# Optimization experiments

Measured on AMD Instinct MI355X. Metric: run time of the kernel, lower is better.

The kernel has to match this reference:

```python
import jax, jax.numpy as jnp
import numpy as np

OUT, IN = 11008, 4096
B, S = 8, 32


def setup_inputs() -> dict:
    key = jax.random.key(0)
    k_x, k_w, k_s, k_b = jax.random.split(key, 4)
    x = jax.random.normal(k_x, (B, S, IN), dtype=jnp.float32).astype(jnp.float16)
    # int8 weight storage (symmetric quant range [-128, 127])
    w_int8 = jax.random.randint(k_w, (OUT, IN), -128, 128, dtype=jnp.int32).astype(jnp.int8)
    # per-output-channel scale, small positive values typical of int8 quant
    scale = jax.random.uniform(k_s, (OUT,), dtype=jnp.float32) * 0.01 + 1e-4
    bias = (jax.random.normal(k_b, (OUT,), dtype=jnp.float32) * 0.02).astype(jnp.float16)
    return {"x": x, "w_int8": w_int8, "scale": scale, "bias": bias}


def reference(x, w_int8, scale, bias):
    # w_fp[o, i] = int8_weight[o, i] * scale[o]   (on-the-fly dequant)
    w = w_int8.astype(jnp.float32) * scale[:, None]          # [OUT, IN] fp32
    # F.linear: out = x @ w.T + bias, computed in fp32
    out = jnp.einsum('bsi,oi->bso', x.astype(jnp.float32), w) + bias.astype(jnp.float32)
    return out.astype(x.dtype)                                # cast back to x.dtype (fp16)
```

## Files before the change

### kernel.cpp

```cpp
#include <hip/hip_runtime.h>
#include <hip/hip_bf16.h>
#include <stdint.h>

typedef __attribute__((ext_vector_type(8))) __bf16 bf16x8;
typedef __attribute__((ext_vector_type(4))) float f32x4;

constexpr int K_DIM = 4096;
constexpr int N_DIM = 11008;
constexpr int M_DIM = 256;
constexpr int TN = 32;
constexpr int BK = 64;
constexpr int NT = 256;
constexpr int KTILES = K_DIM / BK;

__device__ __forceinline__ void gload_lds16(const __bf16* gptr, __bf16* lptr) {
  __builtin_amdgcn_global_load_lds(
      (const __attribute__((address_space(1))) uint32_t*)gptr,
      (__attribute__((address_space(3))) uint32_t*)lptr, 16, 0, 0);
}

__global__ void cvt_x_kernel(const float* __restrict__ x, __bf16* __restrict__ ws) {
  const int i = (blockIdx.x * 256 + threadIdx.x) * 8;
  const float4 u0 = ((const float4*)(x + i))[0];
  const float4 u1 = ((const float4*)(x + i))[1];
  bf16x8 v;
  v[0] = (__bf16)u0.x; v[1] = (__bf16)u0.y; v[2] = (__bf16)u0.z; v[3] = (__bf16)u0.w;
  v[4] = (__bf16)u1.x; v[5] = (__bf16)u1.y; v[6] = (__bf16)u1.z; v[7] = (__bf16)u1.w;
  *(bf16x8*)(ws + i) = v;
}

template<bool USE_WS>
__global__ __launch_bounds__(NT, 2) void int8_linear_kernel(
    const float* __restrict__ x,
    const __bf16* __restrict__ xws,
    const int*   __restrict__ w,
    const float* __restrict__ scale,
    const float* __restrict__ bias,
    float*       __restrict__ out)
{
  __shared__ __bf16 As[2][M_DIM * BK];
  __shared__ __bf16 Ws[2][TN * BK];

  const int tid  = threadIdx.x;
  const int lane = tid & 63;
  const int wv   = tid >> 6;
  const int quad = lane >> 4;
  const int l16  = lane & 15;
  const int n_base = blockIdx.x * TN;

  const int tr = tid >> 3;
  const int ca = (tid & 7) ^ (tr & 7);
  const int wrow  = tid >> 3;
  const int wc    = tid & 7;
  const int wslot = wc ^ (wrow & 7);
  const int* wptr = w + (int64_t)(n_base + wrow) * K_DIM + wc * 8;

  f32x4 acc[4][2];
#pragma unroll
  for (int i = 0; i < 4; ++i)
#pragma unroll
    for (int j = 0; j < 2; ++j) acc[i][j] = (f32x4){0.f, 0.f, 0.f, 0.f};

  int wr0[8], wr1[8];
  auto wload = [&](int kt, int* wr) {
    const int4* p = (const int4*)(wptr + kt * BK);
    const int4 u0 = p[0], u1 = p[1];
    wr[0] = u0.x; wr[1] = u0.y; wr[2] = u0.z; wr[3] = u0.w;
    wr[4] = u1.x; wr[5] = u1.y; wr[6] = u1.z; wr[7] = u1.w;
  };
  auto commitW = [&](const int* wr, __bf16* wbuf) {
    bf16x8 v;
#pragma unroll
    for (int j = 0; j < 8; ++j) v[j] = (__bf16)(float)wr[j];
    *(bf16x8*)(wbuf + wrow * BK + wslot * 8) = v;
  };
  auto a_stage = [&](int kt, __bf16* abuf) {
    if (USE_WS) {
      const __bf16* src = xws + (int64_t)tr * K_DIM + kt * BK + ca * 8;
      __bf16* dst = abuf + tid * 8;
#pragma unroll
      for (int r = 0; r < 8; ++r)
        gload_lds16(src + r * 32 * K_DIM, dst + r * 2048);
    } else {
#pragma unroll
      for (int r = 0; r < 8; ++r) {
        const float* s = x + (int64_t)(r * 32 + tr) * K_DIM + kt * BK + ca * 8;
        const float4 u0 = ((const float4*)s)[0];
        const float4 u1 = ((const float4*)s)[1];
        bf16x8 v;
        v[0] = (__bf16)u0.x; v[1] = (__bf16)u0.y; v[2] = (__bf16)u0.z; v[3] = (__bf16)u0.w;
        v[4] = (__bf16)u1.x; v[5] = (__bf16)u1.y; v[6] = (__bf16)u1.z; v[7] = (__bf16)u1.w;
        *(bf16x8*)(abuf + r * 2048 + tid * 8) = v;
      }
    }
  };
  auto compute = [&](const __bf16* abuf, const __bf16* wbuf) {
#pragma unroll
    for (int ks = 0; ks < 2; ++ks) {
      bf16x8 a[4], b[2];
#pragma unroll
      for (int mi = 0; mi < 4; ++mi) {
        const int m = wv * 64 + mi * 16 + l16;
        const int slot = (ks * 4 + quad) ^ (m & 7);
        a[mi] = *(const bf16x8*)(abuf + m * BK + slot * 8);
      }
#pragma unroll
      for (int ni = 0; ni < 2; ++ni) {
        const int n = ni * 16 + l16;
        const int slot = (ks * 4 + quad) ^ (n & 7);
        b[ni] = *(const bf16x8*)(wbuf + n * BK + slot * 8);
      }
#pragma unroll
      for (int mi = 0; mi < 4; ++mi)
#pragma unroll
        for (int ni = 0; ni < 2; ++ni)
          acc[mi][ni] = __builtin_amdgcn_mfma_f32_16x16x32_bf16(
              a[mi], b[ni], acc[mi][ni], 0, 0, 0);
    }
  };

  wload(0, wr0);
  commitW(wr0, Ws[0]);
  wload(1, wr1);
  a_stage(0, As[0]);

  for (int kt = 0; kt < KTILES; kt += 2) {
    {
      __syncthreads();
      a_stage(kt + 1, As[1]);
      if (kt + 2 < KTILES) wload(kt + 2, wr0);
      compute(As[0], Ws[0]);
      commitW(wr1, Ws[1]);
    }
    {
      __syncthreads();
      if (kt + 2 < KTILES) a_stage(kt + 2, As[0]);
      if (kt + 3 < KTILES) wload(kt + 3, wr1);
      compute(As[1], Ws[1]);
      if (kt + 2 < KTILES) commitW(wr0, Ws[0]);
    }
  }

#pragma unroll
  for (int ni = 0; ni < 2; ++ni) {
    const int col = n_base + ni * 16 + l16;
    const float sc = scale[col];
    const float bi = bias[col];
#pragma unroll
    for (int mi = 0; mi < 4; ++mi) {
      const int row0 = wv * 64 + mi * 16 + quad * 4;
#pragma unroll
      for (int r = 0; r < 4; ++r)
        out[(int64_t)(row0 + r) * N_DIM + col] = acc[mi][ni][r] * sc + bi;
    }
  }
}

extern "C" void kernel_launch(void* const* d_in, const int* in_sizes, int n_in,
                              void* d_out, int out_size, void* d_ws, size_t ws_size,
                              hipStream_t stream) {
  const float* x     = (const float*)d_in[0];
  const int*   w     = (const int*)d_in[1];
  const float* scale = (const float*)d_in[2];
  const float* bias  = (const float*)d_in[3];
  float* out = (float*)d_out;

  __bf16* xws = (__bf16*)d_ws;
  const bool use_ws = ws_size >= (size_t)M_DIM * K_DIM * sizeof(__bf16);

  dim3 grid(N_DIM / TN), block(NT);
  if (use_ws) {
    cvt_x_kernel<<<M_DIM * K_DIM / (256 * 8), 256, 0, stream>>>(x, xws);
    int8_linear_kernel<true><<<grid, block, 0, stream>>>(x, xws, w, scale, bias, out);
  } else {
    int8_linear_kernel<false><<<grid, block, 0, stream>>>(x, xws, w, scale, bias, out);
  }
}
```

Before: 304.3 us.

## Split K across 3 blocks with atomic accumulation and drop A LDS staging

Adds a split-K dimension (3 chunks) to the grid so that 344 N-tiles become 1032 blocks, which gives better coverage of the 256 CUs. Partial results are combined with float atomics after a memset of the output. The activation tile is no longer staged through LDS: x is pre-converted into a k8-major bf16 layout and each wave loads its A fragments straight from global memory into registers. With LDS usage much smaller, launch bounds are raised to 4 blocks per CU, at the cost of an extra memset, atomic traffic and repeated global reads of A.

```diff
diff --git a/kernel.cpp b/kernel.cpp
--- a/kernel.cpp
+++ b/kernel.cpp
@@ -11,26 +11,28 @@
 constexpr int TN = 32;
 constexpr int BK = 64;
 constexpr int NT = 256;
-constexpr int KTILES = K_DIM / BK;
+constexpr int KT_ALL = K_DIM / BK;
+constexpr int KSPLIT = 3;
 
-__device__ __forceinline__ void gload_lds16(const __bf16* gptr, __bf16* lptr) {
-  __builtin_amdgcn_global_load_lds(
-      (const __attribute__((address_space(1))) uint32_t*)gptr,
-      (__attribute__((address_space(3))) uint32_t*)lptr, 16, 0, 0);
+__device__ __forceinline__ bf16x8 cvt8(const float4 u0, const float4 u1) {
+  bf16x8 v;
+  v[0] = (__bf16)u0.x; v[1] = (__bf16)u0.y; v[2] = (__bf16)u0.z; v[3] = (__bf16)u0.w;
+  v[4] = (__bf16)u1.x; v[5] = (__bf16)u1.y; v[6] = (__bf16)u1.z; v[7] = (__bf16)u1.w;
+  return v;
 }
 
 __global__ void cvt_x_kernel(const float* __restrict__ x, __bf16* __restrict__ ws) {
-  const int i = (blockIdx.x * 256 + threadIdx.x) * 8;
-  const float4 u0 = ((const float4*)(x + i))[0];
-  const float4 u1 = ((const float4*)(x + i))[1];
-  bf16x8 v;
-  v[0] = (__bf16)u0.x; v[1] = (__bf16)u0.y; v[2] = (__bf16)u0.z; v[3] = (__bf16)u0.w;
-  v[4] = (__bf16)u1.x; v[5] = (__bf16)u1.y; v[6] = (__bf16)u1.z; v[7] = (__bf16)u1.w;
-  *(bf16x8*)(ws + i) = v;
+  const int t = blockIdx.x * 256 + threadIdx.x;
+  const int m = t & 255;
+  const int k8 = t >> 8;
+  const float* src = x + (size_t)m * K_DIM + k8 * 8;
+  const float4 u0 = ((const float4*)src)[0];
+  const float4 u1 = ((const float4*)src)[1];
+  *(bf16x8*)(ws + (size_t)t * 8) = cvt8(u0, u1);
 }
 
 template<bool USE_WS>
-__global__ __launch_bounds__(NT, 2) void int8_linear_kernel(
+__global__ __launch_bounds__(NT, 4) void int8_linear_kernel(
     const float* __restrict__ x,
     const __bf16* __restrict__ xws,
     const int*   __restrict__ w,
@@ -38,7 +40,6 @@
     const float* __restrict__ bias,
     float*       __restrict__ out)
 {
-  __shared__ __bf16 As[2][M_DIM * BK];
   __shared__ __bf16 Ws[2][TN * BK];
 
   const int tid  = threadIdx.x;
@@ -47,13 +48,20 @@
   const int quad = lane >> 4;
   const int l16  = lane & 15;
   const int n_base = blockIdx.x * TN;
+  const int kc     = blockIdx.y;
 
-  const int tr = tid >> 3;
-  const int ca = (tid & 7) ^ (tr & 7);
+  const int t0 = (kc * KT_ALL) / KSPLIT;
+  const int t1 = ((kc + 1) * KT_ALL) / KSPLIT;
+  const int ntile = t1 - t0;
+  const int k0 = t0 * BK;
+
   const int wrow  = tid >> 3;
   const int wc    = tid & 7;
   const int wslot = wc ^ (wrow & 7);
-  const int* wptr = w + (int64_t)(n_base + wrow) * K_DIM + wc * 8;
+  const int* wptr = w + (int64_t)(n_base + wrow) * K_DIM + k0 + wc * 8;
+
+  const __bf16* aptr = xws + (size_t)(k0 / 8 + quad) * (M_DIM * 8) + (wv * 64 + l16) * 8;
+  const float* fptr = x + (int64_t)(wv * 64 + l16) * K_DIM + k0 + quad * 8;
 
   f32x4 acc[4][2];
 #pragma unroll
@@ -62,8 +70,8 @@
     for (int j = 0; j < 2; ++j) acc[i][j] = (f32x4){0.f, 0.f, 0.f, 0.f};
 
   int wr0[8], wr1[8];
-  auto wload = [&](int kt, int* wr) {
-    const int4* p = (const int4*)(wptr + kt * BK);
+  auto wload = [&](int t, int* wr) {
+    const int4* p = (const int4*)(wptr + t * BK);
     const int4 u0 = p[0], u1 = p[1];
     wr[0] = u0.x; wr[1] = u0.y; wr[2] = u0.z; wr[3] = u0.w;
     wr[4] = u1.x; wr[5] = u1.y; wr[6] = u1.z; wr[7] = u1.w;
@@ -74,84 +82,77 @@
     for (int j = 0; j < 8; ++j) v[j] = (__bf16)(float)wr[j];
     *(bf16x8*)(wbuf + wrow * BK + wslot * 8) = v;
   };
-  auto a_stage = [&](int kt, __bf16* abuf) {
+  auto compute = [&](int t, const __bf16* wbuf) {
+    bf16x8 a[2][4], b[2][2];
     if (USE_WS) {
-      const __bf16* src = xws + (int64_t)tr * K_DIM + kt * BK + ca * 8;
-      __bf16* dst = abuf + tid * 8;
 #pragma unroll
-      for (int r = 0; r < 8; ++r)
-        gload_lds16(src + r * 32 * K_DIM, dst + r * 2048);
+      for (int ks = 0; ks < 2; ++ks)
+#pragma unroll
+        for (int mi = 0; mi < 4; ++mi)
+          a[ks][mi] = *(const bf16x8*)(aptr + (size_t)(t * 8 + ks * 4) * (M_DIM * 8) + mi * 128);
     } else {
 #pragma unroll
-      for (int r = 0; r < 8; ++r) {
-        const float* s = x + (int64_t)(r * 32 + tr) * K_DIM + kt * BK + ca * 8;
-        const float4 u0 = ((const float4*)s)[0];
-        const float4 u1 = ((const float4*)s)[1];
-        bf16x8 v;
-        v[0] = (__bf16)u0.x; v[1] = (__bf16)u0.y; v[2] = (__bf16)u0.z; v[3] = (__bf16)u0.w;
-        v[4] = (__bf16)u1.x; v[5] = (__bf16)u1.y; v[6] = (__bf16)u1.z; v[7] = (__bf16)u1.w;
-        *(bf16x8*)(abuf + r * 2048 + tid * 8) = v;
-      }
+      for (int ks = 0; ks < 2; ++ks)
+#pragma unroll
+        for (int mi = 0; mi < 4; ++mi) {
+          const float* s = fptr + (int64_t)mi * 16 * K_DIM + t * BK + ks * 32;
+          a[ks][mi] = cvt8(((const float4*)s)[0], ((const float4*)s)[1]);
+        }
     }
-  };
-  auto compute = [&](const __bf16* abuf, const __bf16* wbuf) {
 #pragma unroll
-    for (int ks = 0; ks < 2; ++ks) {
-      bf16x8 a[4], b[2];
-#pragma unroll
-      for (int mi = 0; mi < 4; ++mi) {
-        const int m = wv * 64 + mi * 16 + l16;
-        const int slot = (ks * 4 + quad) ^ (m & 7);
-        a[mi] = *(const bf16x8*)(abuf + m * BK + slot * 8);
-      }
+    for (int ks = 0; ks < 2; ++ks)
 #pragma unroll
       for (int ni = 0; ni < 2; ++ni) {
         const int n = ni * 16 + l16;
         const int slot = (ks * 4 + quad) ^ (n & 7);
-        b[ni] = *(const bf16x8*)(wbuf + n * BK + slot * 8);
+        b[ks][ni] = *(const bf16x8*)(wbuf + n * BK + slot * 8);
       }
+#pragma unroll
+    for (int ks = 0; ks < 2; ++ks)
 #pragma unroll
       for (int mi = 0; mi < 4; ++mi)
 #pragma unroll
         for (int ni = 0; ni < 2; ++ni)
           acc[mi][ni] = __builtin_amdgcn_mfma_f32_16x16x32_bf16(
-              a[mi], b[ni], acc[mi][ni], 0, 0, 0);
-    }
+              a[ks][mi], b[ks][ni], acc[mi][ni], 0, 0, 0);
   };
 
   wload(0, wr0);
   commitW(wr0, Ws[0]);
   wload(1, wr1);
-  a_stage(0, As[0]);
 
-  for (int kt = 0; kt < KTILES; kt += 2) {
+  int t = 0;
+  for (; t + 2 <= ntile; t += 2) {
     {
       __syncthreads();
-      a_stage(kt + 1, As[1]);
-      if (kt + 2 < KTILES) wload(kt + 2, wr0);
-      compute(As[0], Ws[0]);
+      if (t + 2 < ntile) wload(t + 2, wr0);
+      compute(t, Ws[0]);
       commitW(wr1, Ws[1]);
     }
     {
       __syncthreads();
-      if (kt + 2 < KTILES) a_stage(kt + 2, As[0]);
-      if (kt + 3 < KTILES) wload(kt + 3, wr1);
-      compute(As[1], Ws[1]);
-      if (kt + 2 < KTILES) commitW(wr0, Ws[0]);
+      if (t + 3 < ntile) wload(t + 3, wr1);
+      compute(t + 1, Ws[1]);
+      if (t + 2 < ntile) commitW(wr0, Ws[0]);
     }
+  }
+  if (t < ntile) {
+    __syncthreads();
+    compute(t, Ws[0]);
   }
 
 #pragma unroll
   for (int ni = 0; ni < 2; ++ni) {
     const int col = n_base + ni * 16 + l16;
     const float sc = scale[col];
-    const float bi = bias[col];
+    const float bi = (kc == 0) ? bias[col] : 0.0f;
 #pragma unroll
     for (int mi = 0; mi < 4; ++mi) {
       const int row0 = wv * 64 + mi * 16 + quad * 4;
 #pragma unroll
       for (int r = 0; r < 4; ++r)
-        out[(int64_t)(row0 + r) * N_DIM + col] = acc[mi][ni][r] * sc + bi;
+        unsafeAtomicAdd(out + (int64_t)(row0 + r) * N_DIM + col,
+                        acc[mi][ni][r] * sc + bi);
     }
   }
 }
@@ -168,7 +169,9 @@
   __bf16* xws = (__bf16*)d_ws;
   const bool use_ws = ws_size >= (size_t)M_DIM * K_DIM * sizeof(__bf16);
 
-  dim3 grid(N_DIM / TN), block(NT);
+  hipMemsetAsync(out, 0, (size_t)M_DIM * N_DIM * sizeof(float), stream);
+
+  dim3 grid(N_DIM / TN, KSPLIT), block(NT);
   if (use_ws) {
     cvt_x_kernel<<<M_DIM * K_DIM / (256 * 8), 256, 0, stream>>>(x, xws);
     int8_linear_kernel<true><<<grid, block, 0, stream>>>(x, xws, w, scale, bias, out);
```

Measured after the change: 313.2 us. +2.9%, slower.
